# Kernel optimization log

Hardware: AMD Instinct MI355X
Metric: run time of the kernel (lower is better)

The kernel has to match this reference:

```python
import jax, jax.numpy as jnp
import numpy as np

DA, DZ, HID, IM = 5, 10, 128, 64


def _encode(x, w1, b1, w2, b2, w3, b3, wd, bd):
    # Conv2D k=4 s=2 'same' (pad 1,1) + ReLU, x3, then flatten + Dense(20)
    dn = ('NHWC', 'HWIO', 'NHWC')
    for w, b in ((w1, b1), (w2, b2), (w3, b3)):
        x = jax.lax.conv_general_dilated(x, w, (2, 2), [(1, 1), (1, 1)], dimension_numbers=dn)
        x = jax.nn.relu(x + b)
    x = x.reshape(x.shape[0], -1)
    return x @ wd + bd


def _lstm(a_in, k, rk, b):
    # keras LSTM, gate order i,f,c,o; stateful step-by-step == scan over shifted seq
    B = a_in.shape[0]
    def step(carry, x):
        h, c = carry
        g = x @ k + h @ rk + b
        gi, gf, gg, go = jnp.split(g, 4, axis=-1)
        c = jax.nn.sigmoid(gf) * c + jax.nn.sigmoid(gi) * jnp.tanh(gg)
        h = jax.nn.sigmoid(go) * jnp.tanh(c)
        return (h, c), h
    z = jnp.zeros((B, HID), a_in.dtype)
    _, hs = jax.lax.scan(step, (z, z), jnp.swapaxes(a_in, 0, 1))
    return hs  # [T, B, HID]


def _forward(images, w1, b1, w2, b2, w3, b3, wd, bd, lk, lrk, lb, wabc, babc):
    B, T = images.shape[0], images.shape[1]
    # encode all frames in one batched pass (per-frame encode is recursion-independent)
    lat = _encode(images.reshape(B * T, IM, IM, 1), w1, b1, w2, b2, w3, b3, wd, bd)
    a_all = lat[:, :DA].reshape(B, T, DA)  # encode() mean split
    # LSTM consumes a_prev: a0=zeros at t=0, then a_{t-1}
    a_in = jnp.concatenate([jnp.zeros((B, 1, DA), a_all.dtype), a_all[:, :-1]], axis=1)
    hs = _lstm(a_in, lk, lrk, lb)  # [T,B,HID]
    abc = hs @ wabc + babc  # [T,B,DZ*DZ+DA*DZ]
    A = abc[..., :DZ * DZ].reshape(T, B, DZ, DZ)
    C = abc[..., DZ * DZ:].reshape(T, B, DA, DZ)

    Q = 0.08 * jnp.eye(DZ, dtype=a_all.dtype)
    R = 0.03 * jnp.eye(DA, dtype=a_all.dtype)
    I = jnp.eye(DZ, dtype=a_all.dtype)
    std_min = 1e-4 * I

    def kf(carry, inp):
        z, P = carry
        At, Ct, at = inp
        z_hat = jnp.einsum('bij,bj->bi', At, z)
        P_hat = At @ P @ jnp.swapaxes(At, -1, -2) + Q
        resid = at - jnp.einsum('bij,bj->bi', Ct, z_hat)
        S = Ct @ P_hat @ jnp.swapaxes(Ct, -1, -2) + R
        K = P_hat @ jnp.swapaxes(Ct, -1, -2) @ jnp.linalg.inv(S)
        pz = z_hat + jnp.einsum('bij,bj->bi', K, resid)
        pP = (I - K @ Ct) @ P_hat
        # note: clamped P_hat is stored, but update() above used the unclamped one
        return (pz, pP), (z_hat, jnp.maximum(P_hat, std_min), pz, pP)

    z0 = jnp.zeros((B, DZ), a_all.dtype)
    P0 = jnp.broadcast_to(I, (B, DZ, DZ))
    _, (z_hat_s, P_hat_s, pz_s, pP_s) = jax.lax.scan(kf, (z0, P0), (A, C, jnp.swapaxes(a_all, 0, 1)))
    last_z, last_P = pz_s[-1], pP_s[-1]

    def rts(carry, inp):
        zs, Ps = carry
        pz_prev, pP_prev, Aj, zhj, Phj = inp
        D = pP_prev @ jnp.swapaxes(Aj, -1, -2) @ jnp.linalg.inv(Phj)
        zn = pz_prev + jnp.einsum('bij,bj->bi', D, zs - zhj)
        Pn = pP_prev + D @ (Ps - Phj) @ jnp.swapaxes(D, -1, -2)
        return (zn, Pn), (zn, Pn)

    # j = T-1 .. 1, reading post[j-1], A[j], z_hat[j], P_hat_clamped[j]
    rev = (pz_s[:-1][::-1], pP_s[:-1][::-1], A[1:][::-1], z_hat_s[1:][::-1], P_hat_s[1:][::-1])
    _, (zsm_r, Psm_r) = jax.lax.scan(rts, (last_z, last_P), rev)
    z_smooth = jnp.swapaxes(zsm_r[::-1], 0, 1)  # [B, T-1, DZ]
    P_smooth = jnp.swapaxes(Psm_r[::-1], 0, 1)  # [B, T-1, DZ, DZ]
    return z_smooth, P_smooth, a_all, A, C, last_z, last_P


def setup_inputs() -> dict:
    key = jax.random.key(0)
    ks = jax.random.split(key, 9)
    B, T = 3, 128
    f = lambda k, shape, s: jax.random.normal(k, shape, jnp.float32) * s
    return {
        'images': jax.random.uniform(ks[0], (B, T, IM, IM, 1), jnp.float32),
        'w1': f(ks[1], (4, 4, 1, 64), 0.25), 'b1': jnp.zeros((64,), jnp.float32),
        'w2': f(ks[2], (4, 4, 64, 128), 0.03), 'b2': jnp.zeros((128,), jnp.float32),
        'w3': f(ks[3], (4, 4, 128, 512), 0.022), 'b3': jnp.zeros((512,), jnp.float32),
        'wd': f(ks[4], (8 * 8 * 512, 20), 0.006), 'bd': jnp.zeros((20,), jnp.float32),
        'lk': f(ks[5], (DA, 4 * HID), 0.3), 'lrk': f(ks[6], (HID, 4 * HID), 0.08),
        'lb': jnp.zeros((4 * HID,), jnp.float32),
        'wabc': f(ks[7], (HID, DZ * DZ + DA * DZ), 0.02),
        'babc': jnp.zeros((DZ * DZ + DA * DZ,), jnp.float32),
    }


def reference(images, w1, b1, w2, b2, w3, b3, wd, bd, lk, lrk, lb, wabc, babc):
    return _forward(images, w1, b1, w2, b2, w3, b3, wd, bd, lk, lrk, lb, wabc, babc)
```

## Files before the change

kernel.cpp:

```cpp
#include <hip/hip_runtime.h>
#include <math.h>

typedef unsigned int   u32;
typedef unsigned short u16;
typedef short bf16x8 __attribute__((ext_vector_type(8)));
typedef float f32x4  __attribute__((ext_vector_type(4)));

#define OUT_ZS    0
#define OUT_PS    3810
#define OUT_AALL  41910
#define OUT_A     43830
#define OUT_C     82230
#define OUT_LASTZ 101430
#define OUT_LASTP 101460

__device__ __forceinline__ float sigm(float x){ return 1.f/(1.f+expf(-x)); }
__device__ __forceinline__ float safed(float d){
    return (fabsf(d) < 1e-30f) ? ((d < 0.f) ? -1e-30f : 1e-30f) : d;
}
__device__ __forceinline__ u16 f2b(float f) {
    union { float f; u32 u; } v; v.f = f;
    u32 r = v.u + 0x7fffu + ((v.u >> 16) & 1u);
    return (u16)(r >> 16);
}
__device__ __forceinline__ float b2f(u16 u) {
    union { u32 x; float f; } v; v.x = ((u32)u) << 16; return v.f;
}
__device__ __forceinline__ u32 packb(float a, float b){ return (u32)f2b(a) | ((u32)f2b(b) << 16); }

__device__ u16   r14_c1[25165824];
__device__ u16   r14_c2[12582912];
__device__ u16   r14_w2h[131072];
__device__ u16   r14_w2l[131072];
__device__ u16   r14_w3h[1048576];
__device__ u16   r14_w3l[1048576];
__device__ float r14_wdT[163840];
__device__ float r20_dpart[7680];
__device__ float r14_hs[49152];
__device__ float r14_zhat[3840];
__device__ float r14_phat[38400];
__device__ float r14_pz[3840];
__device__ float r14_pp[38400];
__device__ float r14_aall[1920];
__device__ float r14_A[38400];
__device__ float r14_C[19200];
__device__ float r14_G[38400];

__global__ __launch_bounds__(256) void conv1_r14(const float* __restrict__ img,
        const float* __restrict__ w1, const float* __restrict__ b1, u16* __restrict__ out)
{
    __shared__ float in_lds[66*66];
    const int f = blockIdx.x, tid = threadIdx.x;
    const int og = tid >> 5, sg = tid & 31;

    for (int i = tid; i < 66*66; i += 256) in_lds[i] = 0.f;
    __syncthreads();
    const float4* src = (const float4*)(img + f*4096);
    for (int i = tid; i < 1024; i += 256) {
        int r = i >> 4, c0 = (i & 15) * 4;
        float4 v = src[i];
        float* dst = &in_lds[(r+1)*66 + c0 + 1];
        dst[0]=v.x; dst[1]=v.y; dst[2]=v.z; dst[3]=v.w;
    }
    float wr[16][8];
    #pragma unroll
    for (int k = 0; k < 16; k++) {
        float4 a = *(const float4*)&w1[k*64 + og*8];
        float4 b = *(const float4*)&w1[k*64 + og*8 + 4];
        wr[k][0]=a.x; wr[k][1]=a.y; wr[k][2]=a.z; wr[k][3]=a.w;
        wr[k][4]=b.x; wr[k][5]=b.y; wr[k][6]=b.z; wr[k][7]=b.w;
    }
    float bias[8];
    #pragma unroll
    for (int j = 0; j < 8; j++) bias[j] = b1[og*8+j];
    __syncthreads();

    for (int yy = 0; yy < 32; yy++) {
        float inv[16];
        #pragma unroll
        for (int ky = 0; ky < 4; ky++)
            #pragma unroll
            for (int kx = 0; kx < 4; kx++)
                inv[ky*4+kx] = in_lds[(2*yy+ky)*66 + 2*sg+kx];
        float acc[8];
        #pragma unroll
        for (int j = 0; j < 8; j++) acc[j] = bias[j];
        #pragma unroll
        for (int k = 0; k < 16; k++)
            #pragma unroll
            for (int j = 0; j < 8; j++) acc[j] += inv[k]*wr[k][j];
        #pragma unroll
        for (int j = 0; j < 8; j++) acc[j] = fmaxf(acc[j], 0.f);
        uint4 pk = make_uint4(packb(acc[0],acc[1]), packb(acc[2],acc[3]),
                              packb(acc[4],acc[5]), packb(acc[6],acc[7]));
        *(uint4*)(out + (f*1024 + yy*32 + sg)*64 + og*8) = pk;
    }
}

__global__ __launch_bounds__(256) void w2t_r14(const float* __restrict__ w2,
        u16* __restrict__ hi, u16* __restrict__ lo)
{
    int idx = blockIdx.x*256 + threadIdx.x;
    if (idx < 131072) {
        int k = idx >> 7, oc = idx & 127;
        float v = w2[idx];
        u16 h = f2b(v);
        hi[oc*1024 + k] = h;
        lo[oc*1024 + k] = f2b(v - b2f(h));
    }
}
__global__ __launch_bounds__(256) void w3t_r14(const float* __restrict__ w3,
        u16* __restrict__ hi, u16* __restrict__ lo)
{
    int idx = blockIdx.x*256 + threadIdx.x;
    if (idx < 1048576) {
        int k = idx >> 9, oc = idx & 511;
        float v = w3[idx];
        u16 h = f2b(v);
        hi[oc*2048 + k] = h;
        lo[oc*2048 + k] = f2b(v - b2f(h));
    }
}
__global__ __launch_bounds__(256) void wdt_r14(const float* __restrict__ wd, float* __restrict__ wdT)
{
    int idx = blockIdx.x*256 + threadIdx.x;
    if (idx < 163840) {
        int j = idx & 32767, d = idx >> 15;
        wdT[d*32768 + j] = wd[j*20 + d];
    }
}

__global__ __launch_bounds__(256) void conv2_r14(const u16* __restrict__ c1b,
        const u16* __restrict__ w2h, const u16* __restrict__ w2l,
        const float* __restrict__ b2, u16* __restrict__ c2b)
{
    __shared__ __align__(16) u16 slab[128*72];
    const int f = blockIdx.x, mc = blockIdx.y, tid = threadIdx.x;
    const int wave = tid >> 6, lane = tid & 63, quad = lane >> 4, ln = lane & 15;

    f32x4 acc[8][2];
    const f32x4 zz = {0.f, 0.f, 0.f, 0.f};
    #pragma unroll
    for (int mt = 0; mt < 8; mt++) { acc[mt][0] = zz; acc[mt][1] = zz; }

    const int sp = tid >> 1;
    const int sy = mc*8 + (sp >> 4), sx = sp & 15;
    const int sic = (tid & 1) * 32;

    for (int kk = 0; kk < 16; kk++) {
        const int ky = kk >> 2, kx = kk & 3;
        __syncthreads();
        {
            int iy = 2*sy - 1 + ky, ix = 2*sx - 1 + kx;
            uint4* d4 = (uint4*)&slab[sp*72 + sic];
            if (iy >= 0 && iy < 32 && ix >= 0 && ix < 32) {
                const uint4* s4 = (const uint4*)&c1b[((f*32 + iy)*32 + ix)*64 + sic];
                d4[0]=s4[0]; d4[1]=s4[1]; d4[2]=s4[2]; d4[3]=s4[3];
            } else {
                uint4 z = make_uint4(0,0,0,0);
                d4[0]=z; d4[1]=z; d4[2]=z; d4[3]=z;
            }
        }
        __syncthreads();
        #pragma unroll
        for (int ks = 0; ks < 2; ks++) {
            bf16x8 af[8];
            #pragma unroll
            for (int mt = 0; mt < 8; mt++)
                af[mt] = *(const bf16x8*)&slab[(mt*16 + ln)*72 + ks*32 + quad*8];
            #pragma unroll
            for (int nt = 0; nt < 2; nt++) {
                const int oc = wave*32 + nt*16 + ln;
                const int kb = kk*64 + ks*32 + quad*8;
                bf16x8 bh = *(const bf16x8*)&w2h[oc*1024 + kb];
                bf16x8 bl = *(const bf16x8*)&w2l[oc*1024 + kb];
                #pragma unroll
                for (int mt = 0; mt < 8; mt++) {
                    acc[mt][nt] = __builtin_amdgcn_mfma_f32_16x16x32_bf16(af[mt], bh, acc[mt][nt], 0,0,0);
                    acc[mt][nt] = __builtin_amdgcn_mfma_f32_16x16x32_bf16(af[mt], bl, acc[mt][nt], 0,0,0);
                }
            }
        }
    }
    #pragma unroll
    for (int nt = 0; nt < 2; nt++) {
        const int oc = wave*32 + nt*16 + ln;
        const float bias = b2[oc];
        #pragma unroll
        for (int mt = 0; mt < 8; mt++)
            #pragma unroll
            for (int r = 0; r < 4; r++) {
                int pix = mc*128 + mt*16 + quad*4 + r;
                c2b[(f*256 + pix)*128 + oc] = f2b(fmaxf(acc[mt][nt][r] + bias, 0.f));
            }
    }
}

__global__ __launch_bounds__(256, 3) void conv3_r21(const u16* __restrict__ c2b,
        const u16* __restrict__ w3h, const u16* __restrict__ w3l,
        const float* __restrict__ b3)
{
    __shared__ __align__(16) u16 slab[2][64*136];
    const int fp = blockIdx.x, ocg = blockIdx.y, tid = threadIdx.x;
    const int wave = tid >> 6, lane = tid & 63, quad = lane >> 4, ln = lane & 15;
    const int wn = ocg*128 + wave*32;

    f32x4 acc[2][4][2];
    const f32x4 zz = {0.f, 0.f, 0.f, 0.f};
    #pragma unroll
    for (int f2 = 0; f2 < 2; f2++)
        #pragma unroll
        for (int mt = 0; mt < 4; mt++) { acc[f2][mt][0] = zz; acc[f2][mt][1] = zz; }

    const int sp = tid >> 2;
    const int sy = sp >> 3, sx = sp & 7;
    const int sic = (tid & 3) * 32;

    for (int kk = 0; kk < 16; kk++) {
        const int ky = kk >> 2, kx = kk & 3;
        const int iy = 2*sy - 1 + ky, ix = 2*sx - 1 + kx;
        const bool vin = (iy >= 0 && iy < 16 && ix >= 0 && ix < 16);
        __syncthreads();
        #pragma unroll
        for (int f2 = 0; f2 < 2; f2++) {
            const int f = fp*2 + f2;
            uint4* d4 = (uint4*)&slab[f2][sp*136 + sic];
            if (vin) {
                const uint4* s4 = (const uint4*)&c2b[((f*16 + iy)*16 + ix)*128 + sic];
                d4[0]=s4[0]; d4[1]=s4[1]; d4[2]=s4[2]; d4[3]=s4[3];
            } else {
                uint4 z = make_uint4(0,0,0,0);
                d4[0]=z; d4[1]=z; d4[2]=z; d4[3]=z;
            }
        }
        __syncthreads();
        #pragma unroll
        for (int ks = 0; ks < 4; ks++) {
            bf16x8 af[2][4];
            #pragma unroll
            for (int f2 = 0; f2 < 2; f2++)
                #pragma unroll
                for (int mt = 0; mt < 4; mt++)
                    af[f2][mt] = *(const bf16x8*)&slab[f2][(mt*16 + ln)*136 + ks*32 + quad*8];
            const int kb = kk*128 + ks*32 + quad*8;
            #pragma unroll
            for (int nt = 0; nt < 2; nt++) {
                const int oc = wn + nt*16 + ln;
                bf16x8 bh = *(const bf16x8*)&w3h[oc*2048 + kb];
                bf16x8 bl = *(const bf16x8*)&w3l[oc*2048 + kb];
                #pragma unroll
                for (int f2 = 0; f2 < 2; f2++)
                    #pragma unroll
                    for (int mt = 0; mt < 4; mt++) {
                        acc[f2][mt][nt] = __builtin_amdgcn_mfma_f32_16x16x32_bf16(af[f2][mt], bh, acc[f2][mt][nt], 0,0,0);
                        acc[f2][mt][nt] = __builtin_amdgcn_mfma_f32_16x16x32_bf16(af[f2][mt], bl, acc[f2][mt][nt], 0,0,0);
                    }
            }
        }
    }

    float pd[2][5];
    #pragma unroll
    for (int f2 = 0; f2 < 2; f2++)
        #pragma unroll
        for (int d = 0; d < 5; d++) pd[f2][d] = 0.f;
    #pragma unroll
    for (int nt = 0; nt < 2; nt++) {
        const int oc = wn + nt*16 + ln;
        const float bias = b3[oc];
        #pragma unroll
        for (int mt = 0; mt < 4; mt++)
            #pragma unroll
            for (int r = 0; r < 4; r++) {
                const int pix = mt*16 + quad*4 + r;
                const float* wp = &r14_wdT[pix*512 + oc];
                const float w0 = wp[0], w1 = wp[32768], w2 = wp[65536],
                            w3v = wp[98304], w4 = wp[131072];
                #pragma unroll
                for (int f2 = 0; f2 < 2; f2++) {
                    const float v = fmaxf(acc[f2][mt][nt][r] + bias, 0.f);
                    pd[f2][0] += v*w0; pd[f2][1] += v*w1; pd[f2][2] += v*w2;
                    pd[f2][3] += v*w3v; pd[f2][4] += v*w4;
                }
            }
    }
    __syncthreads();
    float* red = (float*)slab;
    #pragma unroll
    for (int f2 = 0; f2 < 2; f2++)
        #pragma unroll
        for (int d = 0; d < 5; d++) red[(f2*5+d)*256 + tid] = pd[f2][d];
    __syncthreads();
    for (int st = 128; st > 0; st >>= 1) {
        if (tid < st) {
            #pragma unroll
            for (int q = 0; q < 10; q++) red[q*256+tid] += red[q*256+tid+st];
        }
        __syncthreads();
    }
    if (tid < 10) {
        const int f2 = tid/5, d = tid%5;
        r20_dpart[((fp*2+f2)*4 + ocg)*5 + d] = red[tid*256];
    }
}

__global__ __launch_bounds__(512) void lstm_r22(const float* __restrict__ lk,
        const float* __restrict__ lrk, const float* __restrict__ lb,
        const float* __restrict__ bd, float* __restrict__ dout)
{
    const int b = blockIdx.x, c = threadIdx.x;
    __shared__ float a_lds[640];
    __shared__ float h_lds[128];
    __shared__ float g_lds[512];
    for (int i = c; i < 640; i += 512) {
        const int f = b*128 + i/5, d = i % 5;
        float v = bd[d];
        #pragma unroll
        for (int g = 0; g < 4; g++) v += r20_dpart[f*20 + g*5 + d];
        a_lds[i] = v;
        r14_aall[f*5 + d] = v;
        dout[OUT_AALL + f*5 + d] = v;
    }
    if (c < 128) h_lds[c] = 0.f;
    float wreg[128];
    #pragma unroll
    for (int j = 0; j < 128; j++) wreg[j] = lrk[j*512 + c];
    float lkr[5];
    #pragma unroll
    for (int d = 0; d < 5; d++) lkr[d] = lk[d*512 + c];
    const float gb = lb[c];
    const bool is_gg = (c >= 256 && c < 384);
    float cs = 0.f;
    __syncthreads();
    for (int t = 0; t < 128; t++) {
        float g = gb;
        if (t > 0) {
            #pragma unroll
            for (int d = 0; d < 5; d++) g += a_lds[(t-1)*5 + d] * lkr[d];
        }
        float s0=0.f, s1=0.f, s2=0.f, s3=0.f;
        #pragma unroll
        for (int j = 0; j < 128; j += 4) {
            float4 h4 = *(const float4*)&h_lds[j];
            s0 += h4.x*wreg[j];   s1 += h4.y*wreg[j+1];
            s2 += h4.z*wreg[j+2]; s3 += h4.w*wreg[j+3];
        }
        g += (s0 + s1) + (s2 + s3);
        g_lds[c] = is_gg ? tanhf(g) : sigm(g);
        __syncthreads();
        if (c < 128) {
            float ai = g_lds[c], af_ = g_lds[c+128], ag = g_lds[c+256], ao = g_lds[c+384];
            cs = af_*cs + ai*ag;
            float hn = ao*tanhf(cs);
            h_lds[c] = hn;
            r14_hs[(t*3 + b)*128 + c] = hn;
        }
        __syncthreads();
    }
}

__global__ __launch_bounds__(192) void abc_r14(const float* __restrict__ wabc,
        const float* __restrict__ babc, float* __restrict__ dout)
{
    const int tb = blockIdx.x, c = threadIdx.x;
    __shared__ float h_lds[128];
    if (c < 128) h_lds[c] = r14_hs[tb*128 + c];
    __syncthreads();
    if (c < 150) {
        float s = babc[c];
        for (int j = 0; j < 128; j++) s += h_lds[j]*wabc[j*150 + c];
        if (c < 100) { r14_A[tb*100 + c] = s; dout[OUT_A + tb*100 + c] = s; }
        else         { r14_C[tb*50 + (c-100)] = s; dout[OUT_C + tb*50 + (c-100)] = s; }
    }
}

__global__ __launch_bounds__(128) void kf_r22(float* __restrict__ dout)
{
    const int b = blockIdx.x, tid = threadIdx.x;
    const int i10 = tid/10, j10 = tid%10;
    __shared__ float Ab[2][100], Cb[2][56], avb[2][8];
    __shared__ float z[12], P[100], zh[12], AP[100], Ph[100], resid[8],
                     CPm[52], PCt[52], Ssh[28], Kg[52];

    float rA = 0.f, rC = 0.f, rav = 0.f;
    if (tid < 100) rA  = r14_A[(0*3+b)*100 + tid];
    if (tid < 50)  rC  = r14_C[(0*3+b)*50 + tid];
    if (tid < 5)   rav = r14_aall[(b*128+0)*5 + tid];
    if (tid < 100) P[tid] = (i10==j10) ? 1.f : 0.f;
    if (tid < 10)  z[tid] = 0.f;
    if (tid < 100) Ab[0][tid] = rA;
    if (tid < 50)  Cb[0][tid] = rC;
    if (tid < 5)   avb[0][tid] = rav;
    if (tid < 100) rA  = r14_A[(1*3+b)*100 + tid];
    if (tid < 50)  rC  = r14_C[(1*3+b)*50 + tid];
    if (tid < 5)   rav = r14_aall[(b*128+1)*5 + tid];
    __syncthreads();

    for (int t = 0; t < 128; t++) {
        const int cb = t & 1, nb = cb ^ 1;
        const float* Ax = Ab[cb];
        const float* Cx = Cb[cb];

        if (tid < 100) {
            float s = 0.f;
            #pragma unroll
            for (int k = 0; k < 10; k++) s += Ax[i10*10+k]*P[k*10+j10];
            AP[tid] = s;
        } else if (tid < 110) {
            const int i = tid - 100;
            float s = 0.f;
            #pragma unroll
            for (int k = 0; k < 10; k++) s += Ax[i*10+k]*z[k];
            zh[i] = s;
        }
        __syncthreads();

        if (tid < 100) {
            float s = (i10==j10) ? 0.08f : 0.f;
            #pragma unroll
            for (int k = 0; k < 10; k++) s += AP[i10*10+k]*Ax[j10*10+k];
            Ph[tid] = s;
        } else if (tid < 105) {
            const int c = tid - 100;
            float s = avb[cb][c];
            #pragma unroll
            for (int k = 0; k < 10; k++) s -= Cx[c*10+k]*zh[k];
            resid[c] = s;
        }
        __syncthreads();

        if (tid < 50) {
            const int i = tid/10, j = tid%10;
            float s = 0.f;
            #pragma unroll
            for (int k = 0; k < 10; k++) s += Cx[i*10+k]*Ph[k*10+j];
            CPm[tid] = s;
        } else if (tid >= 64 && tid < 114) {
            const int q = tid-64, i = q/5, j = q%5;
            float s = 0.f;
            #pragma unroll
            for (int k = 0; k < 10; k++) s += Ph[i*10+k]*Cx[j*10+k];
            PCt[q] = s;
        }
        __syncthreads();

        if (tid < 25) {
            const int i = tid/5, j = tid%5;
            float s = (i==j) ? 0.03f : 0.f;
            #pragma unroll
            for (int k = 0; k < 10; k++) s += CPm[i*10+k]*Cx[j*10+k];
            Ssh[tid] = s;
        }
        __syncthreads();

        if (t < 127) {
            if (tid < 100) Ab[nb][tid] = rA;
            if (tid < 50)  Cb[nb][tid] = rC;
            if (tid < 5)   avb[nb][tid] = rav;
            if (t < 126) {
                if (tid < 100) rA  = r14_A[((t+2)*3+b)*100 + tid];
                if (tid < 50)  rC  = r14_C[((t+2)*3+b)*50 + tid];
                if (tid < 5)   rav = r14_aall[(b*128+(t+2))*5 + tid];
            }
        }
        if (tid < 10) {
            float M[5][5], bb[5], pv[5], x[5];
            #pragma unroll
            for (int r = 0; r < 5; r++)
                #pragma unroll
                for (int c = 0; c < 5; c++) M[r][c] = Ssh[c*5+r];
            #pragma unroll
            for (int k = 0; k < 5; k++) bb[k] = PCt[tid*5+k];
            #pragma unroll
            for (int k = 0; k < 5; k++) {
                const float p = 1.f/safed(M[k][k]);
                pv[k] = p;
                #pragma unroll
                for (int r = k+1; r < 5; r++) {
                    const float f = M[r][k]*p;
                    #pragma unroll
                    for (int c = k+1; c < 5; c++) M[r][c] -= f*M[k][c];
                    bb[r] -= f*bb[k];
                }
            }
            #pragma unroll
            for (int k = 4; k >= 0; k--) {
                float s = bb[k];
                #pragma unroll
                for (int c = k+1; c < 5; c++) s -= M[k][c]*x[c];
                x[k] = s*pv[k];
            }
            #pragma unroll
            for (int k = 0; k < 5; k++) Kg[tid*5+k] = x[k];
        }
        __syncthreads();

        if (tid < 100) {
            float s = Ph[tid];
            #pragma unroll
            for (int k = 0; k < 5; k++) s -= Kg[i10*5+k]*CPm[k*10+j10];
            r14_pp[(t*3+b)*100 + tid] = s;
            P[tid] = s;
            r14_phat[(t*3+b)*100 + tid] = fmaxf(Ph[tid], (i10==j10)?1e-4f:0.f);
            if (tid < 10) r14_zhat[(t*3+b)*10 + tid] = zh[tid];
        } else if (tid < 110) {
            const int i = tid - 100;
            float s = zh[i];
            #pragma unroll
            for (int k = 0; k < 5; k++) s += Kg[i*5+k]*resid[k];
            r14_pz[(t*3+b)*10 + i] = s;
            z[i] = s;
        }
        __syncthreads();
    }
    if (tid < 10)  dout[OUT_LASTZ + b*10 + tid]  = z[tid];
    if (tid < 100) dout[OUT_LASTP + b*100 + tid] = P[tid];
}

__global__ __launch_bounds__(256) void ginv_r14()
{
    const int idx = blockIdx.x;
    const int tt = idx/3 + 1, b = idx%3;
    const int tid = threadIdx.x;
    __shared__ float M[10][21];
    __shared__ float A[100];
    __shared__ int piv;
    if (tid < 100) {
        int i = tid/10, j = tid%10;
        M[i][j] = r14_phat[(tt*3+b)*100 + tid];
        M[i][10+j] = (i==j) ? 1.f : 0.f;
        A[tid] = r14_A[(tt*3+b)*100 + tid];
    }
    __syncthreads();
    const int r = tid/20, cc = tid%20;
    for (int k = 0; k < 10; k++) {
        if (tid == 0) {
            int p = k; float best = fabsf(M[k][k]);
            for (int rr = k+1; rr < 10; rr++) {
                float v = fabsf(M[rr][k]);
                if (v > best) { best = v; p = rr; }
            }
            piv = p;
        }
        __syncthreads();
        if (piv != k && tid < 20) {
            float a = M[k][tid], bb = M[piv][tid];
            M[k][tid] = bb; M[piv][tid] = a;
        }
        __syncthreads();
        float pinv = 1.f/safed(M[k][k]);
        float myf = 0.f, rowv = 0.f;
        if (tid < 200) { myf = M[r][k]; rowv = M[k][cc]; }
        __syncthreads();
        if (tid < 200) {
            if (r == k) M[k][cc] = rowv*pinv;
            else        M[r][cc] -= myf*pinv*rowv;
        }
        __syncthreads();
    }
    if (tid < 100) {
        int i = tid/10, j = tid%10;
        float s = 0.f;
        #pragma unroll
        for (int k = 0; k < 10; k++) s += A[k*10+i]*M[k][10+j];
        r14_G[(tt*3+b)*100 + tid] = s;
    }
}

__global__ __launch_bounds__(128) void rts_r22(float* __restrict__ dout)
{
    const int b = blockIdx.x, tid = threadIdx.x;
    const int i10 = tid/10, j10 = tid%10;
    const bool hz = (tid >= 100 && tid < 110);
    const int zi = tid - 100;
    __shared__ float zc[12], Pc[100], D[100], dz[12], T1[100];
    __shared__ float Gtb[2][100], pPb[2][100], phb[2][100], zhb[2][12], pzb[2][12];

    if (tid < 10) zc[tid] = r14_pz[(127*3+b)*10 + tid];
    if (tid < 100) Pc[tid] = r14_pp[(127*3+b)*100 + tid];

    float g0=0.f, p0=0.f, f0=0.f, zr=0.f, pr=0.f;
    if (tid < 100) {
        Gtb[0][tid] = r14_G[(127*3+b)*100 + tid];
        pPb[0][tid] = r14_pp[(126*3+b)*100 + tid];
        phb[0][tid] = r14_phat[(127*3+b)*100 + tid];
    }
    if (hz) {
        zhb[0][zi] = r14_zhat[(127*3+b)*10 + zi];
        pzb[0][zi] = r14_pz[(126*3+b)*10 + zi];
    }
    if (tid < 100) {
        g0 = r14_G[(126*3+b)*100 + tid];
        p0 = r14_pp[(125*3+b)*100 + tid];
        f0 = r14_phat[(126*3+b)*100 + tid];
    }
    if (hz) {
        zr = r14_zhat[(126*3+b)*10 + zi];
        pr = r14_pz[(125*3+b)*10 + zi];
    }
    __syncthreads();

    for (int t = 126; t >= 0; t--) {
        const int cb = (126 - t) & 1, nb = cb ^ 1;

        if (tid < 100) {
            float s = 0.f;
            #pragma unroll
            for (int k = 0; k < 10; k++) s += pPb[cb][i10*10+k]*Gtb[cb][k*10+j10];
            D[tid] = s;
        } else if (tid < 110) {
            dz[zi] = zc[zi] - zhb[cb][zi];
        }
        __syncthreads();

        if (tid < 100) {
            float s = 0.f;
            #pragma unroll
            for (int k = 0; k < 10; k++) s += D[i10*10+k]*(Pc[k*10+j10] - phb[cb][k*10+j10]);
            T1[tid] = s;
        } else if (tid < 110) {
            float s2 = pzb[cb][zi];
            #pragma unroll
            for (int k = 0; k < 10; k++) s2 += D[zi*10+k]*dz[k];
            zc[zi] = s2;
            dout[OUT_ZS + (b*127+t)*10 + zi] = s2;
        }
        if (t > 0) {
            if (tid < 100) { Gtb[nb][tid] = g0; pPb[nb][tid] = p0; phb[nb][tid] = f0; }
            if (hz)        { zhb[nb][zi] = zr; pzb[nb][zi] = pr; }
            if (t > 1) {
                const int s2 = t - 2;
                if (tid < 100) {
                    g0 = r14_G[((s2+1)*3+b)*100 + tid];
                    p0 = r14_pp[(s2*3+b)*100 + tid];
                    f0 = r14_phat[((s2+1)*3+b)*100 + tid];
                }
                if (hz) {
                    zr = r14_zhat[((s2+1)*3+b)*10 + zi];
                    pr = r14_pz[(s2*3+b)*10 + zi];
                }
            }
        }
        __syncthreads();

        if (tid < 100) {
            float s = pPb[cb][tid];
            #pragma unroll
            for (int k = 0; k < 10; k++) s += T1[i10*10+k]*D[j10*10+k];
            dout[OUT_PS + (b*127+t)*100 + tid] = s;
            Pc[tid] = s;
        }
        __syncthreads();
    }
}

extern "C" void kernel_launch(void* const* d_in, const int* in_sizes, int n_in,
                              void* d_out, int out_size, void* d_ws, size_t ws_size,
                              hipStream_t stream)
{
    (void)in_sizes; (void)n_in; (void)out_size; (void)d_ws; (void)ws_size;
    const float* images = (const float*)d_in[0];
    const float* w1   = (const float*)d_in[1];
    const float* b1   = (const float*)d_in[2];
    const float* w2   = (const float*)d_in[3];
    const float* b2   = (const float*)d_in[4];
    const float* w3   = (const float*)d_in[5];
    const float* b3   = (const float*)d_in[6];
    const float* wd   = (const float*)d_in[7];
    const float* bd   = (const float*)d_in[8];
    const float* lk   = (const float*)d_in[9];
    const float* lrk  = (const float*)d_in[10];
    const float* lb   = (const float*)d_in[11];
    const float* wabc = (const float*)d_in[12];
    const float* babc = (const float*)d_in[13];
    float* dout = (float*)d_out;

    u16 *c1p, *c2p, *w2hp, *w2lp, *w3hp, *w3lp;
    float *wdTp;
    hipGetSymbolAddress((void**)&c1p,  HIP_SYMBOL(r14_c1));
    hipGetSymbolAddress((void**)&c2p,  HIP_SYMBOL(r14_c2));
    hipGetSymbolAddress((void**)&w2hp, HIP_SYMBOL(r14_w2h));
    hipGetSymbolAddress((void**)&w2lp, HIP_SYMBOL(r14_w2l));
    hipGetSymbolAddress((void**)&w3hp, HIP_SYMBOL(r14_w3h));
    hipGetSymbolAddress((void**)&w3lp, HIP_SYMBOL(r14_w3l));
    hipGetSymbolAddress((void**)&wdTp, HIP_SYMBOL(r14_wdT));

    conv1_r14<<<dim3(384), dim3(256), 0, stream>>>(images, w1, b1, c1p);
    w2t_r14<<<dim3(512), dim3(256), 0, stream>>>(w2, w2hp, w2lp);
    w3t_r14<<<dim3(4096), dim3(256), 0, stream>>>(w3, w3hp, w3lp);
    wdt_r14<<<dim3(640), dim3(256), 0, stream>>>(wd, wdTp);
    conv2_r14<<<dim3(384, 2), dim3(256), 0, stream>>>(c1p, w2hp, w2lp, b2, c2p);
    conv3_r21<<<dim3(192, 4), dim3(256), 0, stream>>>(c2p, w3hp, w3lp, b3);
    lstm_r22<<<dim3(3), dim3(512), 0, stream>>>(lk, lrk, lb, bd, dout);
    abc_r14<<<dim3(384), dim3(192), 0, stream>>>(wabc, babc, dout);
    kf_r22<<<dim3(3), dim3(128), 0, stream>>>(dout);
    ginv_r14<<<dim3(381), dim3(256), 0, stream>>>();
    rts_r22<<<dim3(3), dim3(128), 0, stream>>>(dout);
}
```

Measured before the change: 823.3 us.

## Process two frames per conv2 block and cut KF step barriers

```diff
diff --git a/kernel.cpp b/kernel.cpp
--- a/kernel.cpp
+++ b/kernel.cpp
@@ -130,18 +130,20 @@
     }
 }
 
-__global__ __launch_bounds__(256) void conv2_r14(const u16* __restrict__ c1b,
+__global__ __launch_bounds__(256) void conv2_r24(const u16* __restrict__ c1b,
         const u16* __restrict__ w2h, const u16* __restrict__ w2l,
         const float* __restrict__ b2, u16* __restrict__ c2b)
 {
-    __shared__ __align__(16) u16 slab[128*72];
-    const int f = blockIdx.x, mc = blockIdx.y, tid = threadIdx.x;
+    __shared__ __align__(16) u16 slab[2][128*72];
+    const int fp = blockIdx.x, mc = blockIdx.y, tid = threadIdx.x;
     const int wave = tid >> 6, lane = tid & 63, quad = lane >> 4, ln = lane & 15;
 
-    f32x4 acc[8][2];
+    f32x4 acc[2][8][2];
     const f32x4 zz = {0.f, 0.f, 0.f, 0.f};
     #pragma unroll
-    for (int mt = 0; mt < 8; mt++) { acc[mt][0] = zz; acc[mt][1] = zz; }
+    for (int f2 = 0; f2 < 2; f2++)
+        #pragma unroll
+        for (int mt = 0; mt < 8; mt++) { acc[f2][mt][0] = zz; acc[f2][mt][1] = zz; }
 
     const int sp = tid >> 1;
     const int sy = mc*8 + (sp >> 4), sx = sp & 15;
@@ -149,11 +151,14 @@
 
     for (int kk = 0; kk < 16; kk++) {
         const int ky = kk >> 2, kx = kk & 3;
-        __syncthreads();
-        {
-            int iy = 2*sy - 1 + ky, ix = 2*sx - 1 + kx;
-            uint4* d4 = (uint4*)&slab[sp*72 + sic];
-            if (iy >= 0 && iy < 32 && ix >= 0 && ix < 32) {
+        const int iy = 2*sy - 1 + ky, ix = 2*sx - 1 + kx;
+        const bool vin = (iy >= 0 && iy < 32 && ix >= 0 && ix < 32);
+        __syncthreads();
+        #pragma unroll
+        for (int f2 = 0; f2 < 2; f2++) {
+            const int f = fp*2 + f2;
+            uint4* d4 = (uint4*)&slab[f2][sp*72 + sic];
+            if (vin) {
                 const uint4* s4 = (const uint4*)&c1b[((f*32 + iy)*32 + ix)*64 + sic];
                 d4[0]=s4[0]; d4[1]=s4[1]; d4[2]=s4[2]; d4[3]=s4[3];
             } else {
@@ -164,10 +169,12 @@
         __syncthreads();
         #pragma unroll
         for (int ks = 0; ks < 2; ks++) {
-            bf16x8 af[8];
-            #pragma unroll
-            for (int mt = 0; mt < 8; mt++)
-                af[mt] = *(const bf16x8*)&slab[(mt*16 + ln)*72 + ks*32 + quad*8];
+            bf16x8 af[2][8];
+            #pragma unroll
+            for (int f2 = 0; f2 < 2; f2++)
+                #pragma unroll
+                for (int mt = 0; mt < 8; mt++)
+                    af[f2][mt] = *(const bf16x8*)&slab[f2][(mt*16 + ln)*72 + ks*32 + quad*8];
             #pragma unroll
             for (int nt = 0; nt < 2; nt++) {
                 const int oc = wave*32 + nt*16 + ln;
@@ -175,10 +182,12 @@
                 bf16x8 bh = *(const bf16x8*)&w2h[oc*1024 + kb];
                 bf16x8 bl = *(const bf16x8*)&w2l[oc*1024 + kb];
                 #pragma unroll
-                for (int mt = 0; mt < 8; mt++) {
-                    acc[mt][nt] = __builtin_amdgcn_mfma_f32_16x16x32_bf16(af[mt], bh, acc[mt][nt], 0,0,0);
-                    acc[mt][nt] = __builtin_amdgcn_mfma_f32_16x16x32_bf16(af[mt], bl, acc[mt][nt], 0,0,0);
-                }
+                for (int f2 = 0; f2 < 2; f2++)
+                    #pragma unroll
+                    for (int mt = 0; mt < 8; mt++) {
+                        acc[f2][mt][nt] = __builtin_amdgcn_mfma_f32_16x16x32_bf16(af[f2][mt], bh, acc[f2][mt][nt], 0,0,0);
+                        acc[f2][mt][nt] = __builtin_amdgcn_mfma_f32_16x16x32_bf16(af[f2][mt], bl, acc[f2][mt][nt], 0,0,0);
+                    }
             }
         }
     }
@@ -187,12 +196,14 @@
         const int oc = wave*32 + nt*16 + ln;
         const float bias = b2[oc];
         #pragma unroll
-        for (int mt = 0; mt < 8; mt++)
-            #pragma unroll
-            for (int r = 0; r < 4; r++) {
-                int pix = mc*128 + mt*16 + quad*4 + r;
-                c2b[(f*256 + pix)*128 + oc] = f2b(fmaxf(acc[mt][nt][r] + bias, 0.f));
-            }
+        for (int f2 = 0; f2 < 2; f2++)
+            #pragma unroll
+            for (int mt = 0; mt < 8; mt++)
+                #pragma unroll
+                for (int r = 0; r < 4; r++) {
+                    int pix = mc*128 + mt*16 + quad*4 + r;
+                    c2b[((fp*2+f2)*256 + pix)*128 + oc] = f2b(fmaxf(acc[f2][mt][nt][r] + bias, 0.f));
+                }
     }
 }
 
@@ -374,13 +385,13 @@
     }
 }
 
-__global__ __launch_bounds__(128) void kf_r22(float* __restrict__ dout)
+__global__ __launch_bounds__(128) void kf_r24(float* __restrict__ dout)
 {
     const int b = blockIdx.x, tid = threadIdx.x;
     const int i10 = tid/10, j10 = tid%10;
     __shared__ float Ab[2][100], Cb[2][56], avb[2][8];
-    __shared__ float z[12], P[100], zh[12], AP[100], Ph[100], resid[8],
-                     CPm[52], PCt[52], Ssh[28], Kg[52];
+    __shared__ float z[12], P[100], zh[12], Ph[100], resid[8],
+                     CPm[52], PCt[52], Kg[52];
 
     float rA = 0.f, rC = 0.f, rav = 0.f;
     if (tid < 100) rA  = r14_A[(0*3+b)*100 + tid];
@@ -402,10 +413,19 @@
         const float* Cx = Cb[cb];
 
         if (tid < 100) {
-            float s = 0.f;
-            #pragma unroll
-            for (int k = 0; k < 10; k++) s += Ax[i10*10+k]*P[k*10+j10];
-            AP[tid] = s;
+            float tk[10];
+            #pragma unroll
+            for (int k = 0; k < 10; k++) tk[k] = 0.f;
+            #pragma unroll
+            for (int l = 0; l < 10; l++) {
+                const float a_il = Ax[i10*10+l];
+                #pragma unroll
+                for (int k = 0; k < 10; k++) tk[k] += a_il * P[l*10+k];
+            }
+            float s = (i10==j10) ? 0.08f : 0.f;
+            #pragma unroll
+            for (int k = 0; k < 10; k++) s += tk[k]*Ax[j10*10+k];
+            Ph[tid] = s;
         } else if (tid < 110) {
             const int i = tid - 100;
             float s = 0.f;
@@ -415,41 +435,24 @@
         }
         __syncthreads();
 
-        if (tid < 100) {
-            float s = (i10==j10) ? 0.08f : 0.f;
-            #pragma unroll
-            for (int k = 0; k < 10; k++) s += AP[i10*10+k]*Ax[j10*10+k];
-            Ph[tid] = s;
-        } else if (tid < 105) {
-            const int c = tid - 100;
-            float s = avb[cb][c];
-            #pragma unroll
-            for (int k = 0; k < 10; k++) s -= Cx[c*10+k]*zh[k];
-            resid[c] = s;
-        }
-        __syncthreads();
-
         if (tid < 50) {
             const int i = tid/10, j = tid%10;
             float s = 0.f;
             #pragma unroll
             for (int k = 0; k < 10; k++) s += Cx[i*10+k]*Ph[k*10+j];
             CPm[tid] = s;
+        } else if (tid < 55) {
+            const int c = tid - 50;
+            float s = avb[cb][c];
+            #pragma unroll
+            for (int k = 0; k < 10; k++) s -= Cx[c*10+k]*zh[k];
+            resid[c] = s;
         } else if (tid >= 64 && tid < 114) {
             const int q = tid-64, i = q/5, j = q%5;
             float s = 0.f;
             #pragma unroll
             for (int k = 0; k < 10; k++) s += Ph[i*10+k]*Cx[j*10+k];
             PCt[q] = s;
-        }
-        __syncthreads();
-
-        if (tid < 25) {
-            const int i = tid/5, j = tid%5;
-            float s = (i==j) ? 0.03f : 0.f;
-            #pragma unroll
-            for (int k = 0; k < 10; k++) s += CPm[i*10+k]*Cx[j*10+k];
-            Ssh[tid] = s;
         }
         __syncthreads();
 
@@ -466,9 +469,14 @@
         if (tid < 10) {
             float M[5][5], bb[5], pv[5], x[5];
             #pragma unroll
-            for (int r = 0; r < 5; r++)
-                #pragma unroll
-                for (int c = 0; c < 5; c++) M[r][c] = Ssh[c*5+r];
+            for (int c = 0; c < 5; c++)
+                #pragma unroll
+                for (int r = 0; r < 5; r++) {
+                    float s = (c==r) ? 0.03f : 0.f;
+                    #pragma unroll
+                    for (int k = 0; k < 10; k++) s += CPm[c*10+k]*Cx[r*10+k];
+                    M[r][c] = s;
+                }
             #pragma unroll
             for (int k = 0; k < 5; k++) bb[k] = PCt[tid*5+k];
             #pragma unroll
@@ -689,11 +697,11 @@
     w2t_r14<<<dim3(512), dim3(256), 0, stream>>>(w2, w2hp, w2lp);
     w3t_r14<<<dim3(4096), dim3(256), 0, stream>>>(w3, w3hp, w3lp);
     wdt_r14<<<dim3(640), dim3(256), 0, stream>>>(wd, wdTp);
-    conv2_r14<<<dim3(384, 2), dim3(256), 0, stream>>>(c1p, w2hp, w2lp, b2, c2p);
+    conv2_r24<<<dim3(192, 2), dim3(256), 0, stream>>>(c1p, w2hp, w2lp, b2, c2p);
     conv3_r21<<<dim3(192, 4), dim3(256), 0, stream>>>(c2p, w3hp, w3lp, b3);
     lstm_r22<<<dim3(3), dim3(512), 0, stream>>>(lk, lrk, lb, bd, dout);
     abc_r14<<<dim3(384), dim3(192), 0, stream>>>(wabc, babc, dout);
-    kf_r22<<<dim3(3), dim3(128), 0, stream>>>(dout);
+    kf_r24<<<dim3(3), dim3(128), 0, stream>>>(dout);
     ginv_r14<<<dim3(381), dim3(256), 0, stream>>>();
     rts_r22<<<dim3(3), dim3(128), 0, stream>>>(dout);
 }
```

New measurement: 963.8 us. 1.17x slower.
